# Performance work log

Measured on AMD Instinct MI355X. Metric: run time of the kernel, lower is better.

The kernel has to match this reference:

```python
import jax, jax.numpy as jnp
import numpy as np

KERNEL_SIZE = 5


def setup_inputs() -> dict:
    key = jax.random.key(0)
    k1, k2, k3 = jax.random.split(key, 3)
    B, H, W = 32, 512, 512
    f = jax.random.uniform(k1, (B, H, W), dtype=jnp.float32)          # distribution function, non-negative
    K = jax.random.normal(k2, (KERNEL_SIZE, KERNEL_SIZE, H, W), dtype=jnp.float32) * 0.01  # per-pixel kernels
    dt = jax.random.uniform(k3, (B,), dtype=jnp.float32) * 0.1        # per-batch timestep
    return {"f": f, "K": K, "dt": dt}


def reference(f, K, dt):
    # f: (B,H,W); K: (k,k,H,W) position-dependent (unshared) kernels; dt: (B,)
    # Equivalent to: patches = unfold(pad(f)); df = einsum('bkv,kv->bv', patches, K.reshape(k*k,-1))
    # Implemented as a sum over the k*k kernel taps of shifted slices (avoids the
    # B*k^2*H*W patches tensor; loop is over the fixed kernel footprint, not data dims).
    k = K.shape[0]
    B, H, W = f.shape
    pl, pr = k // 2, (k - 1) // 2  # matches pad_size = (k//2, (k-1)//2)*2
    f_pad = jnp.pad(f, ((0, 0), (pl, pr), (pl, pr)))  # 'zeros' padding_mode
    df = jnp.zeros_like(f)
    for i in range(k):
        for j in range(k):
            df = df + f_pad[:, i:i + H, j:j + W] * K[i, j]
    out = f + df * dt[:, None, None]
    return jnp.maximum(out, 0.0)  # ensure_non_negative_f clamp
```

## Files before the change

kernel.cpp:

```cpp
#include <hip/hip_runtime.h>

#define H 512
#define W 512
#define BATCH 32
#define KS 5
#define B_CHUNK 8
#define LROW 520
#define LBUF (6 * LROW)

typedef const __attribute__((address_space(1))) void gv_t;
typedef __attribute__((address_space(3))) void lv_t;

__device__ __forceinline__ void async_cp16(const float* src, float* lds_dst) {
    __builtin_amdgcn_global_load_lds((gv_t*)src, (lv_t*)lds_dst, 16, 0, 0);
}

__device__ __forceinline__ void prefetch_tile(const float* __restrict__ fb,
                                              float* ldsbuf,
                                              int wave, int lane, int h0) {
#pragma unroll
    for (int k = 0; k < 3; ++k) {
        const int c    = wave * 3 + k;
        const int r    = c >> 1;
        const int half = c & 1;
        const int gr   = h0 - 2 + r;
        if (gr >= 0 && gr < H) {
            const float* src = fb + gr * W + half * 256 + lane * 4;
            float* dst = ldsbuf + r * LROW + 4 + half * 256;
            async_cp16(src, dst);
        }
    }
}

__global__ __launch_bounds__(256, 2) void op2d_kernel(
    const float* __restrict__ f,
    const float* __restrict__ K,
    const float* __restrict__ dt,
    float* __restrict__ out)
{
    __shared__ float lds[2 * LBUF];

    const int tid  = threadIdx.x;
    const int lane = tid & 63;
    const int wave = tid >> 6;
    const int w0   = (tid & 127) * 4;
    const int lr   = tid >> 7;
    const int h0   = blockIdx.y * 2;
    const int h    = h0 + lr;
    const int chunk = blockIdx.x;

#pragma unroll
    for (int i = tid; i < 2 * LBUF; i += 256) lds[i] = 0.f;

    float4 Kv[25];
#pragma unroll
    for (int t = 0; t < 25; ++t) {
        Kv[t] = *reinterpret_cast<const float4*>(K + (t * H + h) * W + w0);
    }

    __syncthreads();

    const float* fb0 = f + (size_t)(chunk * B_CHUNK) * H * W;
    prefetch_tile(fb0, lds, wave, lane, h0);

#pragma unroll
    for (int bb = 0; bb < B_CHUNK; ++bb) {
        __syncthreads();

        const int cur = bb & 1;
        if (bb + 1 < B_CHUNK) {
            prefetch_tile(fb0 + (size_t)(bb + 1) * H * W,
                          lds + (1 - cur) * LBUF, wave, lane, h0);
        }

        const int b   = chunk * B_CHUNK + bb;
        const float dtb = dt[b];
        const float* Lb = lds + cur * LBUF;

        float acc0 = 0.f, acc1 = 0.f, acc2 = 0.f, acc3 = 0.f;
        float fc0 = 0.f, fc1 = 0.f, fc2 = 0.f, fc3 = 0.f;

#pragma unroll
        for (int i = 0; i < KS; ++i) {
            const int tr = lr + i;
            const float* row = Lb + tr * LROW + w0;
            const float4 ra = *reinterpret_cast<const float4*>(row);
            const float4 rb = *reinterpret_cast<const float4*>(row + 4);
            const float4 rc = *reinterpret_cast<const float4*>(row + 8);
            const float buf[12] = { ra.x, ra.y, ra.z, ra.w,
                                    rb.x, rb.y, rb.z, rb.w,
                                    rc.x, rc.y, rc.z, rc.w };

            if (i == 2) { fc0 = rb.x; fc1 = rb.y; fc2 = rb.z; fc3 = rb.w; }

#pragma unroll
            for (int j = 0; j < KS; ++j) {
                const float4 kv = Kv[i * KS + j];
                acc0 += kv.x * buf[j + 2];
                acc1 += kv.y * buf[j + 3];
                acc2 += kv.z * buf[j + 4];
                acc3 += kv.w * buf[j + 5];
            }
        }

        float4 o;
        o.x = fmaxf(fc0 + acc0 * dtb, 0.f);
        o.y = fmaxf(fc1 + acc1 * dtb, 0.f);
        o.z = fmaxf(fc2 + acc2 * dtb, 0.f);
        o.w = fmaxf(fc3 + acc3 * dtb, 0.f);
        *reinterpret_cast<float4*>(out + ((size_t)b * H + h) * W + w0) = o;
    }
}

extern "C" void kernel_launch(void* const* d_in, const int* in_sizes, int n_in,
                              void* d_out, int out_size, void* d_ws, size_t ws_size,
                              hipStream_t stream) {
    const float* f  = (const float*)d_in[0];
    const float* K  = (const float*)d_in[1];
    const float* dt = (const float*)d_in[2];
    float* out = (float*)d_out;

    dim3 block(256);
    dim3 grid(BATCH / B_CHUNK, H / 2);
    op2d_kernel<<<grid, block, 0, stream>>>(f, K, dt, out);
}
```

Baseline: 124.1 us.

## Load all batch tiles at once and stream kernel taps per row

Replaces the double-buffered per-batch pipeline with a single bulk async load of four batch tiles into LDS, one wave per batch. Kernel weights are now loaded one row of taps at a time and reused across the four batches held in register accumulators, instead of keeping all 25 taps live. This lowers register pressure so occupancy can rise to three blocks per CU, and outputs use nontemporal stores. The trade-offs are that the loads no longer overlap compute within a block, and K is read twice as often overall because the batch chunk is halved.

After: 125.3 us. No clear change (+1.0%).

```diff
diff --git a/kernel.cpp b/kernel.cpp
--- a/kernel.cpp
+++ b/kernel.cpp
@@ -4,111 +4,107 @@
 #define W 512
 #define BATCH 32
 #define KS 5
-#define B_CHUNK 8
+#define B_CHUNK 4
 #define LROW 520
-#define LBUF (6 * LROW)
+#define LTILE (6 * LROW)
+#define LDS_FLOATS (B_CHUNK * LTILE)
 
 typedef const __attribute__((address_space(1))) void gv_t;
 typedef __attribute__((address_space(3))) void lv_t;
+typedef float nf4 __attribute__((ext_vector_type(4)));
 
 __device__ __forceinline__ void async_cp16(const float* src, float* lds_dst) {
     __builtin_amdgcn_global_load_lds((gv_t*)src, (lv_t*)lds_dst, 16, 0, 0);
 }
 
-__device__ __forceinline__ void prefetch_tile(const float* __restrict__ fb,
-                                              float* ldsbuf,
-                                              int wave, int lane, int h0) {
-#pragma unroll
-    for (int k = 0; k < 3; ++k) {
-        const int c    = wave * 3 + k;
-        const int r    = c >> 1;
-        const int half = c & 1;
-        const int gr   = h0 - 2 + r;
-        if (gr >= 0 && gr < H) {
-            const float* src = fb + gr * W + half * 256 + lane * 4;
-            float* dst = ldsbuf + r * LROW + 4 + half * 256;
-            async_cp16(src, dst);
-        }
-    }
-}
-
-__global__ __launch_bounds__(256, 2) void op2d_kernel(
+__global__ __launch_bounds__(256, 3) void op2d_kernel(
     const float* __restrict__ f,
     const float* __restrict__ K,
     const float* __restrict__ dt,
     float* __restrict__ out)
 {
-    __shared__ float lds[2 * LBUF];
+    __shared__ float lds[LDS_FLOATS];
 
-    const int tid  = threadIdx.x;
-    const int lane = tid & 63;
-    const int wave = tid >> 6;
-    const int w0   = (tid & 127) * 4;
-    const int lr   = tid >> 7;
-    const int h0   = blockIdx.y * 2;
-    const int h    = h0 + lr;
+    const int tid   = threadIdx.x;
+    const int lane  = tid & 63;
+    const int wave  = tid >> 6;
+    const int w0    = (tid & 127) * 4;
+    const int lr    = tid >> 7;
     const int chunk = blockIdx.x;
+    const int h0    = blockIdx.y * 2;
+    const int h     = h0 + lr;
 
 #pragma unroll
-    for (int i = tid; i < 2 * LBUF; i += 256) lds[i] = 0.f;
-
-    float4 Kv[25];
-#pragma unroll
-    for (int t = 0; t < 25; ++t) {
-        Kv[t] = *reinterpret_cast<const float4*>(K + (t * H + h) * W + w0);
-    }
-
+    for (int idx = tid; idx < LDS_FLOATS; idx += 256) lds[idx] = 0.f;
     __syncthreads();
 
-    const float* fb0 = f + (size_t)(chunk * B_CHUNK) * H * W;
-    prefetch_tile(fb0, lds, wave, lane, h0);
+    {
+        const int b  = wave;
+        const int bg = chunk * B_CHUNK + b;
+        const float* fb = f + (size_t)bg * H * W;
+#pragma unroll
+        for (int k = 0; k < 12; ++k) {
+            const int r    = k >> 1;
+            const int half = k & 1;
+            const int gr   = h0 - 2 + r;
+            if (gr >= 0 && gr < H) {
+                const float* src = fb + (size_t)gr * W + half * 256 + lane * 4;
+                float* dst = lds + b * LTILE + r * LROW + 4 + half * 256;
+                async_cp16(src, dst);
+            }
+        }
+    }
+    __syncthreads();
+
+    float acc[B_CHUNK][4];
+#pragma unroll
+    for (int b = 0; b < B_CHUNK; ++b)
+#pragma unroll
+        for (int p = 0; p < 4; ++p) acc[b][p] = 0.f;
+
+    float fc[B_CHUNK][4];
 
 #pragma unroll
-    for (int bb = 0; bb < B_CHUNK; ++bb) {
-        __syncthreads();
-
-        const int cur = bb & 1;
-        if (bb + 1 < B_CHUNK) {
-            prefetch_tile(fb0 + (size_t)(bb + 1) * H * W,
-                          lds + (1 - cur) * LBUF, wave, lane, h0);
+    for (int i = 0; i < KS; ++i) {
+        float4 Kv[KS];
+#pragma unroll
+        for (int j = 0; j < KS; ++j) {
+            Kv[j] = *reinterpret_cast<const float4*>(
+                K + ((size_t)(i * KS + j) * H + h) * W + w0);
         }
 
-        const int b   = chunk * B_CHUNK + bb;
-        const float dtb = dt[b];
-        const float* Lb = lds + cur * LBUF;
-
-        float acc0 = 0.f, acc1 = 0.f, acc2 = 0.f, acc3 = 0.f;
-        float fc0 = 0.f, fc1 = 0.f, fc2 = 0.f, fc3 = 0.f;
-
 #pragma unroll
-        for (int i = 0; i < KS; ++i) {
-            const int tr = lr + i;
-            const float* row = Lb + tr * LROW + w0;
+        for (int b = 0; b < B_CHUNK; ++b) {
+            const float* row = lds + b * LTILE + (lr + i) * LROW + w0;
             const float4 ra = *reinterpret_cast<const float4*>(row);
             const float4 rb = *reinterpret_cast<const float4*>(row + 4);
             const float4 rc = *reinterpret_cast<const float4*>(row + 8);
             const float buf[12] = { ra.x, ra.y, ra.z, ra.w,
                                     rb.x, rb.y, rb.z, rb.w,
                                     rc.x, rc.y, rc.z, rc.w };
-
-            if (i == 2) { fc0 = rb.x; fc1 = rb.y; fc2 = rb.z; fc3 = rb.w; }
+            if (i == 2) { fc[b][0] = rb.x; fc[b][1] = rb.y;
+                          fc[b][2] = rb.z; fc[b][3] = rb.w; }
+#pragma unroll
+            for (int j = 0; j < KS; ++j) {
+                acc[b][0] += Kv[j].x * buf[j + 2];
+                acc[b][1] += Kv[j].y * buf[j + 3];
+                acc[b][2] += Kv[j].z * buf[j + 4];
+                acc[b][3] += Kv[j].w * buf[j + 5];
+            }
+        }
+    }
 
 #pragma unroll
-            for (int j = 0; j < KS; ++j) {
-                const float4 kv = Kv[i * KS + j];
-                acc0 += kv.x * buf[j + 2];
-                acc1 += kv.y * buf[j + 3];
-                acc2 += kv.z * buf[j + 4];
-                acc3 += kv.w * buf[j + 5];
-            }
-        }
-
-        float4 o;
-        o.x = fmaxf(fc0 + acc0 * dtb, 0.f);
-        o.y = fmaxf(fc1 + acc1 * dtb, 0.f);
-        o.z = fmaxf(fc2 + acc2 * dtb, 0.f);
-        o.w = fmaxf(fc3 + acc3 * dtb, 0.f);
-        *reinterpret_cast<float4*>(out + ((size_t)b * H + h) * W + w0) = o;
+    for (int b = 0; b < B_CHUNK; ++b) {
+        const int bg = chunk * B_CHUNK + b;
+        const float dtb = dt[bg];
+        nf4 o;
+        o.x = fmaxf(fc[b][0] + acc[b][0] * dtb, 0.f);
+        o.y = fmaxf(fc[b][1] + acc[b][1] * dtb, 0.f);
+        o.z = fmaxf(fc[b][2] + acc[b][2] * dtb, 0.f);
+        o.w = fmaxf(fc[b][3] + acc[b][3] * dtb, 0.f);
+        __builtin_nontemporal_store(o,
+            reinterpret_cast<nf4*>(out + ((size_t)bg * H + h) * W + w0));
     }
 }
 
```
